# Kernel optimization log

Measured on AMD Instinct MI355X. Metric: run time of the kernel, lower is better.

Reference implementation:

```python
import jax, jax.numpy as jnp
import numpy as np

B, N, S, D1, D2 = 8, 8192, 2048, 128, 256
MLP = [256, 128]
IN_CH = D1 + D2
EPS_INTERP = 1e-8
EPS_BN = 1e-5


def setup_inputs() -> dict:
    key = jax.random.key(0)
    ks = jax.random.split(key, 12)
    inp = {
        "xyz1": jax.random.normal(ks[0], (B, 3, N), dtype=jnp.float32),
        "xyz2": jax.random.normal(ks[1], (B, 3, S), dtype=jnp.float32),
        "points1": jax.random.normal(ks[2], (B, D1, N), dtype=jnp.float32),
        "points2": jax.random.normal(ks[3], (B, D2, S), dtype=jnp.float32),
    }
    # Conv1d(k=1) weights are [out, in]; BN has gamma/beta per channel.
    last = IN_CH
    for i, oc in enumerate(MLP):
        inp[f"W{i}"] = jax.random.normal(ks[4 + 2 * i], (oc, last), dtype=jnp.float32) * (1.0 / np.sqrt(last))
        inp[f"b{i}"] = jnp.zeros((oc,), dtype=jnp.float32)
        inp[f"g{i}"] = jnp.ones((oc,), dtype=jnp.float32)
        inp[f"be{i}"] = jnp.zeros((oc,), dtype=jnp.float32)
        last = oc
    return inp


def _interpolate(xyz1, xyz2, points2):
    # xyz1: [B,3,N] -> [B,N,3]; xyz2: [B,3,S] -> [B,S,3]; points2: [B,D2,S] -> [B,S,D2]
    x1 = jnp.transpose(xyz1, (0, 2, 1))
    x2 = jnp.transpose(xyz2, (0, 2, 1))
    p2 = jnp.transpose(points2, (0, 2, 1))
    # squared distances [B,N,S]
    dists = (jnp.sum(x1 * x1, -1)[:, :, None]
             - 2.0 * jnp.einsum("bnc,bsc->bns", x1, x2)
             + jnp.sum(x2 * x2, -1)[:, None, :])
    neg_d, idx = jax.lax.top_k(-dists, 3)         # 3 nearest neighbors
    d = -neg_d                                     # [B,N,3]
    recip = 1.0 / (d + EPS_INTERP)
    weight = recip / jnp.sum(recip, axis=2, keepdims=True)
    gathered = jax.vmap(lambda p, i: p[i])(p2, idx)   # [B,N,3,D2]
    return jnp.sum(gathered * weight[..., None], axis=2)  # [B,N,D2]


def _conv_bn_relu(x, W, b, g, be):
    # x: [B,C,N]; 1x1 conv == channel GEMM
    y = jnp.einsum("oc,bcn->bon", W, x) + b[None, :, None]
    mean = jnp.mean(y, axis=(0, 2), keepdims=True)
    var = jnp.mean((y - mean) ** 2, axis=(0, 2), keepdims=True)  # biased, torch BN train
    y = (y - mean) * jax.lax.rsqrt(var + EPS_BN)
    y = y * g[None, :, None] + be[None, :, None]
    return jax.nn.relu(y)


def reference(xyz1, xyz2, points1, points2, W0, b0, g0, be0, W1, b1, g1, be1):
    interp = _interpolate(xyz1, xyz2, points2)               # [B,N,D2]
    p1 = jnp.transpose(points1, (0, 2, 1))                    # [B,N,D1]
    new_points = jnp.concatenate([p1, interp], axis=-1)       # [B,N,D1+D2]
    new_points = jnp.transpose(new_points, (0, 2, 1))         # [B,D1+D2,N]
    new_points = _conv_bn_relu(new_points, W0, b0, g0, be0)
    new_points = _conv_bn_relu(new_points, W1, b1, g1, be1)
    return new_points
```

## Files before the change

### kernel.cpp

```cpp
#include <hip/hip_runtime.h>

typedef unsigned short ushort_t;
typedef __bf16 bf16x8 __attribute__((ext_vector_type(8)));
typedef float floatx4 __attribute__((ext_vector_type(4)));

#define B_ 8
#define N_ 8192
#define S_ 2048
#define D1_ 128
#define D2_ 256
#define INCH_ 384
#define M_ 65536
#define G2_NBLK 512

#define ASYNC_CP16(g, l)                                                  \
  __builtin_amdgcn_global_load_lds(                                       \
      (const __attribute__((address_space(1))) void*)(g),                 \
      (__attribute__((address_space(3))) void*)(l), 16, 0, 0)

constexpr size_t OFF_STATS = 0;
constexpr size_t OFF_W0B   = 8192;
constexpr size_t OFF_W1B   = 204800;
constexpr size_t OFF_X2P   = 270336;
constexpr size_t OFF_P2T   = 532480;
constexpr size_t OFF_XC    = 8921088;
constexpr size_t OFF_Y1    = 59252736;

__device__ __forceinline__ ushort_t f2bf(float f) {
  __bf16 h = (__bf16)f;
  union { __bf16 h; ushort_t u; } v;
  v.h = h;
  return v.u;
}
__device__ __forceinline__ float bf2f(ushort_t h) {
  return __uint_as_float(((unsigned int)h) << 16);
}

__device__ __forceinline__ void ins3(float e, int s,
                                     float& c0, float& c1, float& c2,
                                     int& i0, int& i1, int& i2) {
  bool l0 = e < c0, l1 = e < c1, l2 = e < c2;
  float nf0 = fminf(e, c0);
  float nf1 = __builtin_amdgcn_fmed3f(e, c0, c1);
  float nf2 = __builtin_amdgcn_fmed3f(e, c1, c2);
  i2 = l1 ? i1 : (l2 ? s : i2);
  i1 = l0 ? i0 : (l1 ? s : i1);
  i0 = l0 ? s : i0;
  c0 = nf0; c1 = nf1; c2 = nf2;
}

__global__ __launch_bounds__(256) void k_prep(const float* __restrict__ W0,
                                              const float* __restrict__ W1,
                                              const float* __restrict__ xyz2,
                                              ushort_t* __restrict__ W0b,
                                              ushort_t* __restrict__ W1b,
                                              float4* __restrict__ x2p) {
  int i = blockIdx.x * 256 + threadIdx.x;
  if (i < 98304) {
    W0b[i] = f2bf(W0[i]);
  } else if (i < 131072) {
    W1b[i - 98304] = f2bf(W1[i - 98304]);
  } else {
    int idx = i - 131072;
    int b = idx >> 11, s = idx & (S_ - 1);
    const float* base = xyz2 + (size_t)b * 3 * S_;
    float x = base[s], y = base[S_ + s], z = base[2 * S_ + s];
    x2p[idx] = make_float4(x, y, z, 0.5f * (x * x + y * y + z * z));
  }
}

__global__ void k_tr_p2(const float* __restrict__ P2, ushort_t* __restrict__ p2t) {
  __shared__ float t[32][33];
  int b = blockIdx.z;
  int s0 = blockIdx.x * 32;
  int c0 = blockIdx.y * 32;
  int tx = threadIdx.x, ty = threadIdx.y;
#pragma unroll
  for (int j = 0; j < 4; j++) {
    int c = c0 + ty + j * 8;
    t[ty + j * 8][tx] = P2[((size_t)b * D2_ + c) * S_ + s0 + tx];
  }
  __syncthreads();
#pragma unroll
  for (int j = 0; j < 4; j++) {
    int s = s0 + ty + j * 8;
    p2t[((size_t)b * S_ + s) * D2_ + c0 + tx] = f2bf(t[tx][ty + j * 8]);
  }
}

__global__ void k_tr_p1(const float* __restrict__ P1, ushort_t* __restrict__ Xc) {
  __shared__ float t[32][33];
  int b = blockIdx.z;
  int n0 = blockIdx.x * 32;
  int c0 = blockIdx.y * 32;
  int tx = threadIdx.x, ty = threadIdx.y;
#pragma unroll
  for (int j = 0; j < 4; j++) {
    int c = c0 + ty + j * 8;
    t[ty + j * 8][tx] = P1[((size_t)b * D1_ + c) * N_ + n0 + tx];
  }
  __syncthreads();
#pragma unroll
  for (int j = 0; j < 4; j++) {
    int n = n0 + ty + j * 8;
    Xc[((size_t)b * N_ + n) * INCH_ + c0 + tx] = f2bf(t[tx][ty + j * 8]);
  }
}

__global__ __launch_bounds__(512, 8) void k_knn(const float* __restrict__ xyz1,
                                                const float4* __restrict__ x2p,
                                                const ushort_t* __restrict__ p2t,
                                                ushort_t* __restrict__ Xc) {
  __shared__ float4 xs[8 * 289];
  __shared__ float wsh[64 * 3];
  __shared__ int   ish[64 * 3];
  int t = threadIdx.x;
  int q0 = blockIdx.x * 64;
  int b = q0 >> 13;
  int n0 = q0 & (N_ - 1);
  for (int l = t; l < S_; l += 512)
    xs[(l >> 8) * 289 + (l & 255)] = x2p[(size_t)b * S_ + l];
  int sub = t & 7;
  int qg = t >> 3;
  int n = n0 + qg;
  float qx = xyz1[((size_t)b * 3 + 0) * N_ + n];
  float qy = xyz1[((size_t)b * 3 + 1) * N_ + n];
  float qz = xyz1[((size_t)b * 3 + 2) * N_ + n];
  float nrm1 = qx * qx + qy * qy + qz * qz;
  __syncthreads();
  const float4* bp = xs + sub * 289;
  float k0 = 3e38f, k1 = 3e38f, k2 = 3e38f, k3 = 3e38f;
#pragma unroll 4
  for (int i = 0; i < 256; ++i) {
    float4 P = bp[i];
    float e = fmaf(-qx, P.x, fmaf(-qy, P.y, fmaf(-qz, P.z, P.w)));
    float dd = fmaf(2.f, e, nrm1);
    unsigned int kb = (__float_as_uint(dd) & 0xFFFFFF00u) | (unsigned int)i;
    float k = __uint_as_float(kb);
    float n0_ = fminf(k, k0);
    float n1_ = __builtin_amdgcn_fmed3f(k, k0, k1);
    float n2_ = __builtin_amdgcn_fmed3f(k, k1, k2);
    float n3_ = __builtin_amdgcn_fmed3f(k, k2, k3);
    k0 = n0_; k1 = n1_; k2 = n2_; k3 = n3_;
  }
  float ed[4];
  int   si[4];
  {
    float kk[4] = {k0, k1, k2, k3};
#pragma unroll
    for (int c = 0; c < 4; ++c) {
      int loc = (int)(__float_as_uint(kk[c]) & 255u);
      float4 P = bp[loc];
      float e = fmaf(-qx, P.x, fmaf(-qy, P.y, fmaf(-qz, P.z, P.w)));
      ed[c] = fmaf(2.f, e, nrm1);
      si[c] = (sub << 8) + loc;
    }
  }
  float c0 = 3e38f, c1 = 3e38f, c2 = 3e38f;
  int i0 = 0, i1 = 0, i2 = 0;
#pragma unroll
  for (int c = 0; c < 4; ++c) ins3(ed[c], si[c], c0, c1, c2, i0, i1, i2);
#pragma unroll
  for (int d = 1; d < 8; d <<= 1) {
    float e0 = __shfl_xor(c0, d); int s0 = __shfl_xor(i0, d);
    float e1 = __shfl_xor(c1, d); int s1 = __shfl_xor(i1, d);
    float e2 = __shfl_xor(c2, d); int s2 = __shfl_xor(i2, d);
    ins3(e0, s0, c0, c1, c2, i0, i1, i2);
    ins3(e1, s1, c0, c1, c2, i0, i1, i2);
    ins3(e2, s2, c0, c1, c2, i0, i1, i2);
  }
  if (sub == 0) {
    float r0 = 1.f / (c0 + 1e-8f);
    float r1 = 1.f / (c1 + 1e-8f);
    float r2 = 1.f / (c2 + 1e-8f);
    float rs = 1.f / (r0 + r1 + r2);
    wsh[qg * 3 + 0] = r0 * rs; wsh[qg * 3 + 1] = r1 * rs; wsh[qg * 3 + 2] = r2 * rs;
    ish[qg * 3 + 0] = i0; ish[qg * 3 + 1] = i1; ish[qg * 3 + 2] = i2;
  }
  __syncthreads();
  int lane = t & 63, grp = t >> 6;
  size_t sbase2 = (size_t)b * S_;
#pragma unroll 2
  for (int it = 0; it < 8; ++it) {
    int ql = it * 8 + grp;
    int q = q0 + ql;
    float w0 = wsh[ql * 3 + 0], w1 = wsh[ql * 3 + 1], w2 = wsh[ql * 3 + 2];
    int j0 = ish[ql * 3 + 0], j1 = ish[ql * 3 + 1], j2 = ish[ql * 3 + 2];
    ushort4 a0 = *(const ushort4*)&p2t[(sbase2 + j0) * D2_ + lane * 4];
    ushort4 a1 = *(const ushort4*)&p2t[(sbase2 + j1) * D2_ + lane * 4];
    ushort4 a2 = *(const ushort4*)&p2t[(sbase2 + j2) * D2_ + lane * 4];
    ushort4 o;
    o.x = f2bf(w0 * bf2f(a0.x) + w1 * bf2f(a1.x) + w2 * bf2f(a2.x));
    o.y = f2bf(w0 * bf2f(a0.y) + w1 * bf2f(a1.y) + w2 * bf2f(a2.y));
    o.z = f2bf(w0 * bf2f(a0.z) + w1 * bf2f(a1.z) + w2 * bf2f(a2.z));
    o.w = f2bf(w0 * bf2f(a0.w) + w1 * bf2f(a1.w) + w2 * bf2f(a2.w));
    *(ushort4*)&Xc[(size_t)q * INCH_ + D1_ + lane * 4] = o;
  }
}

__global__ __launch_bounds__(512) void k_gemm1(const ushort_t* __restrict__ A,
                                               const ushort_t* __restrict__ Bw,
                                               ushort_t* __restrict__ Cc,
                                               float* __restrict__ sum,
                                               float* __restrict__ ssq) {
  __shared__ __align__(16) ushort_t As[128 * 32];
  __shared__ __align__(16) ushort_t Bs[256 * 32];
  const int tid = threadIdx.x;
  const int m0 = blockIdx.x * 128;
  const int wave = tid >> 6;
  const int wuni = __builtin_amdgcn_readfirstlane(wave);
  const int lane = tid & 63;
  const int quad = lane >> 4;
  const int l16 = lane & 15;
  const int wrow = (wave >> 2) * 64;
  const int wcol = (wave & 3) * 64;
  const int arow = tid >> 2, aseg = tid & 3;
  floatx4 acc[4][4];
#pragma unroll
  for (int i = 0; i < 4; i++)
#pragma unroll
    for (int j = 0; j < 4; j++) acc[i][j] = (floatx4){0.f, 0.f, 0.f, 0.f};

  for (int k0 = 0; k0 < INCH_; k0 += 32) {
    ASYNC_CP16(&A[(size_t)(m0 + arow) * INCH_ + k0 + aseg * 8], &As[wuni * 512]);
#pragma unroll
    for (int it = 0; it < 2; it++) {
      int l = tid + it * 512;
      int row = l >> 2, seg = l & 3;
      ASYNC_CP16(&Bw[(size_t)row * INCH_ + k0 + seg * 8], &Bs[it * 4096 + wuni * 512]);
    }
    __syncthreads();
    bf16x8 af[4], bfr[4];
#pragma unroll
    for (int mt = 0; mt < 4; mt++) af[mt] = *(const bf16x8*)&As[(wrow + mt * 16 + l16) * 32 + quad * 8];
#pragma unroll
    for (int nt = 0; nt < 4; nt++) bfr[nt] = *(const bf16x8*)&Bs[(wcol + nt * 16 + l16) * 32 + quad * 8];
#pragma unroll
    for (int mt = 0; mt < 4; mt++)
#pragma unroll
      for (int nt = 0; nt < 4; nt++)
        acc[mt][nt] = __builtin_amdgcn_mfma_f32_16x16x32_bf16(af[mt], bfr[nt], acc[mt][nt], 0, 0, 0);
    __syncthreads();
  }
#pragma unroll
  for (int mt = 0; mt < 4; mt++) {
#pragma unroll
    for (int i = 0; i < 4; i++) {
      int row = m0 + wrow + mt * 16 + quad * 4 + i;
#pragma unroll
      for (int nt = 0; nt < 4; nt++) {
        int col = wcol + nt * 16 + l16;
        Cc[(size_t)row * 256 + col] = f2bf(acc[mt][nt][i]);
      }
    }
  }
#pragma unroll
  for (int nt = 0; nt < 4; nt++) {
    float s = 0.f, s2 = 0.f;
#pragma unroll
    for (int mt = 0; mt < 4; mt++)
#pragma unroll
      for (int i = 0; i < 4; i++) {
        float v = acc[mt][nt][i];
        s += v;
        s2 = fmaf(v, v, s2);
      }
    s += __shfl_xor(s, 16);  s2 += __shfl_xor(s2, 16);
    s += __shfl_xor(s, 32);  s2 += __shfl_xor(s2, 32);
    if (quad == 0) {
      int col = wcol + nt * 16 + l16;
      atomicAdd(&sum[col], s);
      atomicAdd(&ssq[col], s2);
    }
  }
}

__global__ __launch_bounds__(256, 2) void k_gemm2o(const ushort_t* __restrict__ Y1,
                                                   const ushort_t* __restrict__ Bw,
                                                   const float* __restrict__ sum0,
                                                   const float* __restrict__ ssq0,
                                                   const float* __restrict__ g0,
                                                   const float* __restrict__ be0,
                                                   const float* __restrict__ g1,
                                                   const float* __restrict__ be1,
                                                   float* __restrict__ sum1,
                                                   float* __restrict__ ssq1,
                                                   unsigned int* __restrict__ barcnt,
                                                   float* __restrict__ out) {
  __shared__ __align__(16) char ubuf[64 * 129 * 4];
  __shared__ float scs[256], shs[256];
  ushort_t* As = (ushort_t*)ubuf;
  ushort_t* Bs = (ushort_t*)(ubuf + 8192);
  float* tb = (float*)ubuf;
  const int tid = threadIdx.x;
  const int m0 = blockIdx.x * 128;
  const int b = m0 >> 13;
  const int n0 = m0 & (N_ - 1);
  const int wave = tid >> 6;
  const int wuni = __builtin_amdgcn_readfirstlane(wave);
  const int lane = tid & 63;
  const int quad = lane >> 4;
  const int l16 = lane & 15;
  const int wrow = (wave >> 1) * 64;
  const int wcol = (wave & 1) * 64;
  {
    float mean = sum0[tid] * (1.f / 65536.f);
    float var = ssq0[tid] * (1.f / 65536.f) - mean * mean;
    float sc = rsqrtf(var + 1e-5f) * g0[tid];
    scs[tid] = sc;
    shs[tid] = be0[tid] - mean * sc;
  }
  floatx4 acc[4][4];
#pragma unroll
  for (int i = 0; i < 4; i++)
#pragma unroll
    for (int j = 0; j < 4; j++) acc[i][j] = (floatx4){0.f, 0.f, 0.f, 0.f};
  __syncthreads();

  for (int k0 = 0; k0 < 256; k0 += 32) {
#pragma unroll
    for (int it = 0; it < 2; it++) {
      int l = tid + it * 256;
      int row = l >> 2, seg = l & 3;
      ASYNC_CP16(&Bw[(size_t)row * 256 + k0 + seg * 8], &Bs[it * 2048 + wuni * 512]);
    }
#pragma unroll
    for (int it = 0; it < 2; it++) {
      int l = tid + it * 256;
      int row = l >> 2, seg = l & 3;
      ushort4 y01 = *(const ushort4*)&Y1[(size_t)(m0 + row) * 256 + k0 + seg * 8];
      ushort4 y23 = *(const ushort4*)&Y1[(size_t)(m0 + row) * 256 + k0 + seg * 8 + 4];
      int c = k0 + seg * 8;
      ushort4 o0, o1;
      o0.x = f2bf(fmaxf(fmaf(bf2f(y01.x), scs[c + 0], shs[c + 0]), 0.f));
      o0.y = f2bf(fmaxf(fmaf(bf2f(y01.y), scs[c + 1], shs[c + 1]), 0.f));
      o0.z = f2bf(fmaxf(fmaf(bf2f(y01.z), scs[c + 2], shs[c + 2]), 0.f));
      o0.w = f2bf(fmaxf(fmaf(bf2f(y01.w), scs[c + 3], shs[c + 3]), 0.f));
      o1.x = f2bf(fmaxf(fmaf(bf2f(y23.x), scs[c + 4], shs[c + 4]), 0.f));
      o1.y = f2bf(fmaxf(fmaf(bf2f(y23.y), scs[c + 5], shs[c + 5]), 0.f));
      o1.z = f2bf(fmaxf(fmaf(bf2f(y23.z), scs[c + 6], shs[c + 6]), 0.f));
      o1.w = f2bf(fmaxf(fmaf(bf2f(y23.w), scs[c + 7], shs[c + 7]), 0.f));
      *(ushort4*)&As[row * 32 + seg * 8] = o0;
      *(ushort4*)&As[row * 32 + seg * 8 + 4] = o1;
    }
    __syncthreads();
    bf16x8 af[4], bfr[4];
#pragma unroll
    for (int mt = 0; mt < 4; mt++) af[mt] = *(const bf16x8*)&As[(wrow + mt * 16 + l16) * 32 + quad * 8];
#pragma unroll
    for (int nt = 0; nt < 4; nt++) bfr[nt] = *(const bf16x8*)&Bs[(wcol + nt * 16 + l16) * 32 + quad * 8];
#pragma unroll
    for (int mt = 0; mt < 4; mt++)
#pragma unroll
      for (int nt = 0; nt < 4; nt++)
        acc[mt][nt] = __builtin_amdgcn_mfma_f32_16x16x32_bf16(af[mt], bfr[nt], acc[mt][nt], 0, 0, 0);
    __syncthreads();
  }
#pragma unroll
  for (int nt = 0; nt < 4; nt++) {
    float s = 0.f, s2 = 0.f;
#pragma unroll
    for (int mt = 0; mt < 4; mt++)
#pragma unroll
      for (int i = 0; i < 4; i++) {
        float v = acc[mt][nt][i];
        s += v;
        s2 = fmaf(v, v, s2);
      }
    s += __shfl_xor(s, 16);  s2 += __shfl_xor(s2, 16);
    s += __shfl_xor(s, 32);  s2 += __shfl_xor(s2, 32);
    if (quad == 0) {
      int col = wcol + nt * 16 + l16;
      atomicAdd(&sum1[col], s);
      atomicAdd(&ssq1[col], s2);
    }
  }

  __syncthreads();
  if (tid == 0) {
    __hip_atomic_fetch_add(barcnt, 1u, __ATOMIC_ACQ_REL, __HIP_MEMORY_SCOPE_AGENT);
    while (__hip_atomic_load(barcnt, __ATOMIC_ACQUIRE, __HIP_MEMORY_SCOPE_AGENT)
           < (unsigned)G2_NBLK) {
      __builtin_amdgcn_s_sleep(8);
    }
  }
  __syncthreads();

  if (tid < 128) {
    float sv = __hip_atomic_load(&sum1[tid], __ATOMIC_RELAXED, __HIP_MEMORY_SCOPE_AGENT);
    float qv = __hip_atomic_load(&ssq1[tid], __ATOMIC_RELAXED, __HIP_MEMORY_SCOPE_AGENT);
    float mean = sv * (1.f / 65536.f);
    float var = qv * (1.f / 65536.f) - mean * mean;
    float sc = rsqrtf(var + 1e-5f) * g1[tid];
    scs[tid] = sc;
    shs[tid] = be1[tid] - mean * sc;
  }
  __syncthreads();

  const int mych = wrow >> 6;
#pragma unroll
  for (int c2 = 0; c2 < 2; ++c2) {
    if (mych == c2) {
#pragma unroll
      for (int mt = 0; mt < 4; mt++)
#pragma unroll
        for (int i = 0; i < 4; i++) {
          int rl = mt * 16 + quad * 4 + i;
#pragma unroll
          for (int nt = 0; nt < 4; nt++) {
            int col = wcol + nt * 16 + l16;
            float v = fmaxf(fmaf(acc[mt][nt][i], scs[col], shs[col]), 0.f);
            tb[rl * 129 + col] = v;
          }
        }
    }
    __syncthreads();
#pragma unroll
    for (int it = 0; it < 32; ++it) {
      int idx = it * 256 + tid;
      int j = idx & 63, c = idx >> 6;
      out[((size_t)(b * 128 + c)) * N_ + n0 + c2 * 64 + j] = tb[j * 129 + c];
    }
    __syncthreads();
  }
}

extern "C" void kernel_launch(void* const* d_in, const int* in_sizes, int n_in,
                              void* d_out, int out_size, void* d_ws, size_t ws_size,
                              hipStream_t stream) {
  const float* xyz1    = (const float*)d_in[0];
  const float* xyz2    = (const float*)d_in[1];
  const float* points1 = (const float*)d_in[2];
  const float* points2 = (const float*)d_in[3];
  const float* W0 = (const float*)d_in[4];
  const float* g0 = (const float*)d_in[6];
  const float* be0 = (const float*)d_in[7];
  const float* W1 = (const float*)d_in[8];
  const float* g1 = (const float*)d_in[10];
  const float* be1 = (const float*)d_in[11];
  float* out = (float*)d_out;
  char* ws = (char*)d_ws;

  float* sum0   = (float*)(ws + OFF_STATS);
  float* ssq0   = sum0 + 256;
  float* sum1   = sum0 + 512;
  float* ssq1   = sum0 + 640;
  unsigned int* barcnt = (unsigned int*)(sum0 + 768);
  ushort_t* W0b = (ushort_t*)(ws + OFF_W0B);
  ushort_t* W1b = (ushort_t*)(ws + OFF_W1B);
  float4* x2p   = (float4*)(ws + OFF_X2P);
  ushort_t* p2t = (ushort_t*)(ws + OFF_P2T);
  ushort_t* Xc  = (ushort_t*)(ws + OFF_XC);
  ushort_t* Y1b = (ushort_t*)(ws + OFF_Y1);

  hipMemsetAsync(ws + OFF_STATS, 0, 6144, stream);
  k_prep<<<576, 256, 0, stream>>>(W0, W1, xyz2, W0b, W1b, x2p);
  k_tr_p2<<<dim3(64, 8, 8), dim3(32, 8), 0, stream>>>(points2, p2t);
  k_tr_p1<<<dim3(256, 4, 8), dim3(32, 8), 0, stream>>>(points1, Xc);
  k_knn<<<1024, 512, 0, stream>>>(xyz1, x2p, p2t, Xc);
  k_gemm1<<<512, 512, 0, stream>>>(Xc, W0b, Y1b, sum0, ssq0);
  k_gemm2o<<<G2_NBLK, 256, 0, stream>>>(Y1b, W1b, sum0, ssq0, g0, be0,
                                        g1, be1, sum1, ssq1, barcnt, out);
}
```

Baseline: 269.4 us.

## Replace in-kernel grid barrier with separate BN-apply kernel and smaller GEMM tiles

The second GEMM no longer spins on a global atomic barrier to get the final BN statistics. It writes pre-BN results as a transposed bf16 buffer (reusing the Xc workspace), and a new elementwise kernel applies BN and ReLU to produce the fp32 output. GEMM tiles are halved to 64 rows with 1024 blocks and launch bounds raised for occupancy. This removes the barrier wait and the co-residency requirement, but adds a bf16 intermediate round trip through global memory, an extra launch, and an extra bf16 rounding before BN.

```diff
diff --git a/kernel.cpp b/kernel.cpp
--- a/kernel.cpp
+++ b/kernel.cpp
@@ -11,7 +11,6 @@
 #define D2_ 256
 #define INCH_ 384
 #define M_ 65536
-#define G2_NBLK 512
 
 #define ASYNC_CP16(g, l)                                                  \
   __builtin_amdgcn_global_load_lds(                                       \
@@ -275,25 +274,22 @@
   }
 }
 
-__global__ __launch_bounds__(256, 2) void k_gemm2o(const ushort_t* __restrict__ Y1,
+__global__ __launch_bounds__(256, 4) void k_gemm2t(const ushort_t* __restrict__ Y1,
                                                    const ushort_t* __restrict__ Bw,
                                                    const float* __restrict__ sum0,
                                                    const float* __restrict__ ssq0,
                                                    const float* __restrict__ g0,
                                                    const float* __restrict__ be0,
-                                                   const float* __restrict__ g1,
-                                                   const float* __restrict__ be1,
+                                                   ushort_t* __restrict__ Y2t,
                                                    float* __restrict__ sum1,
-                                                   float* __restrict__ ssq1,
-                                                   unsigned int* __restrict__ barcnt,
-                                                   float* __restrict__ out) {
+                                                   float* __restrict__ ssq1) {
   __shared__ __align__(16) char ubuf[64 * 129 * 4];
   __shared__ float scs[256], shs[256];
   ushort_t* As = (ushort_t*)ubuf;
-  ushort_t* Bs = (ushort_t*)(ubuf + 8192);
+  ushort_t* Bs = (ushort_t*)(ubuf + 4096);
   float* tb = (float*)ubuf;
   const int tid = threadIdx.x;
-  const int m0 = blockIdx.x * 128;
+  const int m0 = blockIdx.x * 64;
   const int b = m0 >> 13;
   const int n0 = m0 & (N_ - 1);
   const int wave = tid >> 6;
@@ -301,7 +297,7 @@
   const int lane = tid & 63;
   const int quad = lane >> 4;
   const int l16 = lane & 15;
-  const int wrow = (wave >> 1) * 64;
+  const int wrow = (wave >> 1) * 32;
   const int wcol = (wave & 1) * 64;
   {
     float mean = sum0[tid] * (1.f / 65536.f);
@@ -310,13 +306,14 @@
     scs[tid] = sc;
     shs[tid] = be0[tid] - mean * sc;
   }
-  floatx4 acc[4][4];
-#pragma unroll
-  for (int i = 0; i < 4; i++)
+  floatx4 acc[2][4];
+#pragma unroll
+  for (int i = 0; i < 2; i++)
 #pragma unroll
     for (int j = 0; j < 4; j++) acc[i][j] = (floatx4){0.f, 0.f, 0.f, 0.f};
   __syncthreads();
 
+  const int arow = tid >> 2, aseg = tid & 3;
   for (int k0 = 0; k0 < 256; k0 += 32) {
 #pragma unroll
     for (int it = 0; it < 2; it++) {
@@ -324,13 +321,10 @@
       int row = l >> 2, seg = l & 3;
       ASYNC_CP16(&Bw[(size_t)row * 256 + k0 + seg * 8], &Bs[it * 2048 + wuni * 512]);
     }
-#pragma unroll
-    for (int it = 0; it < 2; it++) {
-      int l = tid + it * 256;
-      int row = l >> 2, seg = l & 3;
-      ushort4 y01 = *(const ushort4*)&Y1[(size_t)(m0 + row) * 256 + k0 + seg * 8];
-      ushort4 y23 = *(const ushort4*)&Y1[(size_t)(m0 + row) * 256 + k0 + seg * 8 + 4];
-      int c = k0 + seg * 8;
+    {
+      ushort4 y01 = *(const ushort4*)&Y1[(size_t)(m0 + arow) * 256 + k0 + aseg * 8];
+      ushort4 y23 = *(const ushort4*)&Y1[(size_t)(m0 + arow) * 256 + k0 + aseg * 8 + 4];
+      int c = k0 + aseg * 8;
       ushort4 o0, o1;
       o0.x = f2bf(fmaxf(fmaf(bf2f(y01.x), scs[c + 0], shs[c + 0]), 0.f));
       o0.y = f2bf(fmaxf(fmaf(bf2f(y01.y), scs[c + 1], shs[c + 1]), 0.f));
@@ -340,17 +334,17 @@
       o1.y = f2bf(fmaxf(fmaf(bf2f(y23.y), scs[c + 5], shs[c + 5]), 0.f));
       o1.z = f2bf(fmaxf(fmaf(bf2f(y23.z), scs[c + 6], shs[c + 6]), 0.f));
       o1.w = f2bf(fmaxf(fmaf(bf2f(y23.w), scs[c + 7], shs[c + 7]), 0.f));
-      *(ushort4*)&As[row * 32 + seg * 8] = o0;
-      *(ushort4*)&As[row * 32 + seg * 8 + 4] = o1;
+      *(ushort4*)&As[arow * 32 + aseg * 8] = o0;
+      *(ushort4*)&As[arow * 32 + aseg * 8 + 4] = o1;
     }
     __syncthreads();
-    bf16x8 af[4], bfr[4];
-#pragma unroll
-    for (int mt = 0; mt < 4; mt++) af[mt] = *(const bf16x8*)&As[(wrow + mt * 16 + l16) * 32 + quad * 8];
+    bf16x8 af[2], bfr[4];
+#pragma unroll
+    for (int mt = 0; mt < 2; mt++) af[mt] = *(const bf16x8*)&As[(wrow + mt * 16 + l16) * 32 + quad * 8];
 #pragma unroll
     for (int nt = 0; nt < 4; nt++) bfr[nt] = *(const bf16x8*)&Bs[(wcol + nt * 16 + l16) * 32 + quad * 8];
 #pragma unroll
-    for (int mt = 0; mt < 4; mt++)
+    for (int mt = 0; mt < 2; mt++)
 #pragma unroll
       for (int nt = 0; nt < 4; nt++)
         acc[mt][nt] = __builtin_amdgcn_mfma_f32_16x16x32_bf16(af[mt], bfr[nt], acc[mt][nt], 0, 0, 0);
@@ -360,7 +354,7 @@
   for (int nt = 0; nt < 4; nt++) {
     float s = 0.f, s2 = 0.f;
 #pragma unroll
-    for (int mt = 0; mt < 4; mt++)
+    for (int mt = 0; mt < 2; mt++)
 #pragma unroll
       for (int i = 0; i < 4; i++) {
         float v = acc[mt][nt][i];
@@ -375,53 +369,62 @@
       atomicAdd(&ssq1[col], s2);
     }
   }
-
-  __syncthreads();
-  if (tid == 0) {
-    __hip_atomic_fetch_add(barcnt, 1u, __ATOMIC_ACQ_REL, __HIP_MEMORY_SCOPE_AGENT);
-    while (__hip_atomic_load(barcnt, __ATOMIC_ACQUIRE, __HIP_MEMORY_SCOPE_AGENT)
-           < (unsigned)G2_NBLK) {
-      __builtin_amdgcn_s_sleep(8);
-    }
-  }
-  __syncthreads();
-
+#pragma unroll
+  for (int mt = 0; mt < 2; mt++)
+#pragma unroll
+    for (int i = 0; i < 4; i++) {
+      int rl = wrow + mt * 16 + quad * 4 + i;
+#pragma unroll
+      for (int nt = 0; nt < 4; nt++) {
+        int col = wcol + nt * 16 + l16;
+        tb[rl * 129 + col] = acc[mt][nt][i];
+      }
+    }
+  __syncthreads();
+#pragma unroll
+  for (int it = 0; it < 8; ++it) {
+    int idx = it * 256 + tid;
+    int c = idx >> 4;
+    int j4 = (idx & 15) * 4;
+    ushort4 v;
+    v.x = f2bf(tb[(j4 + 0) * 129 + c]);
+    v.y = f2bf(tb[(j4 + 1) * 129 + c]);
+    v.z = f2bf(tb[(j4 + 2) * 129 + c]);
+    v.w = f2bf(tb[(j4 + 3) * 129 + c]);
+    *(ushort4*)&Y2t[((size_t)(b * 128 + c)) * N_ + n0 + j4] = v;
+  }
+}
+
+__global__ __launch_bounds__(256) void k_out2(const ushort_t* __restrict__ Y2t,
+                                              const float* __restrict__ sum1,
+                                              const float* __restrict__ ssq1,
+                                              const float* __restrict__ g1,
+                                              const float* __restrict__ be1,
+                                              float* __restrict__ out) {
+  __shared__ float sc1[128], sh1[128];
+  int tid = threadIdx.x;
   if (tid < 128) {
-    float sv = __hip_atomic_load(&sum1[tid], __ATOMIC_RELAXED, __HIP_MEMORY_SCOPE_AGENT);
-    float qv = __hip_atomic_load(&ssq1[tid], __ATOMIC_RELAXED, __HIP_MEMORY_SCOPE_AGENT);
-    float mean = sv * (1.f / 65536.f);
-    float var = qv * (1.f / 65536.f) - mean * mean;
+    float mean = sum1[tid] * (1.f / 65536.f);
+    float var = ssq1[tid] * (1.f / 65536.f) - mean * mean;
     float sc = rsqrtf(var + 1e-5f) * g1[tid];
-    scs[tid] = sc;
-    shs[tid] = be1[tid] - mean * sc;
-  }
-  __syncthreads();
-
-  const int mych = wrow >> 6;
-#pragma unroll
-  for (int c2 = 0; c2 < 2; ++c2) {
-    if (mych == c2) {
-#pragma unroll
-      for (int mt = 0; mt < 4; mt++)
-#pragma unroll
-        for (int i = 0; i < 4; i++) {
-          int rl = mt * 16 + quad * 4 + i;
-#pragma unroll
-          for (int nt = 0; nt < 4; nt++) {
-            int col = wcol + nt * 16 + l16;
-            float v = fmaxf(fmaf(acc[mt][nt][i], scs[col], shs[col]), 0.f);
-            tb[rl * 129 + col] = v;
-          }
-        }
-    }
-    __syncthreads();
-#pragma unroll
-    for (int it = 0; it < 32; ++it) {
-      int idx = it * 256 + tid;
-      int j = idx & 63, c = idx >> 6;
-      out[((size_t)(b * 128 + c)) * N_ + n0 + c2 * 64 + j] = tb[j * 129 + c];
-    }
-    __syncthreads();
+    sc1[tid] = sc;
+    sh1[tid] = be1[tid] - mean * sc;
+  }
+  __syncthreads();
+#pragma unroll
+  for (int it = 0; it < 4; ++it) {
+    int fid = (it * 2048 + blockIdx.x) * 256 + tid;
+    int r = fid >> 11;
+    int c = r & 127;
+    int n4 = (fid & 2047) * 4;
+    ushort4 y = *(const ushort4*)&Y2t[((size_t)r << 13) + n4];
+    float sc = sc1[c], sh = sh1[c];
+    float4 v;
+    v.x = fmaxf(fmaf(bf2f(y.x), sc, sh), 0.f);
+    v.y = fmaxf(fmaf(bf2f(y.y), sc, sh), 0.f);
+    v.z = fmaxf(fmaf(bf2f(y.z), sc, sh), 0.f);
+    v.w = fmaxf(fmaf(bf2f(y.w), sc, sh), 0.f);
+    *(float4*)&out[((size_t)r << 13) + n4] = v;
   }
 }
 
@@ -445,13 +448,13 @@
   float* ssq0   = sum0 + 256;
   float* sum1   = sum0 + 512;
   float* ssq1   = sum0 + 640;
-  unsigned int* barcnt = (unsigned int*)(sum0 + 768);
   ushort_t* W0b = (ushort_t*)(ws + OFF_W0B);
   ushort_t* W1b = (ushort_t*)(ws + OFF_W1B);
   float4* x2p   = (float4*)(ws + OFF_X2P);
   ushort_t* p2t = (ushort_t*)(ws + OFF_P2T);
   ushort_t* Xc  = (ushort_t*)(ws + OFF_XC);
   ushort_t* Y1b = (ushort_t*)(ws + OFF_Y1);
+  ushort_t* Y2t = (ushort_t*)(ws + OFF_XC);
 
   hipMemsetAsync(ws + OFF_STATS, 0, 6144, stream);
   k_prep<<<576, 256, 0, stream>>>(W0, W1, xyz2, W0b, W1b, x2p);
@@ -459,6 +462,7 @@
   k_tr_p1<<<dim3(256, 4, 8), dim3(32, 8), 0, stream>>>(points1, Xc);
   k_knn<<<1024, 512, 0, stream>>>(xyz1, x2p, p2t, Xc);
   k_gemm1<<<512, 512, 0, stream>>>(Xc, W0b, Y1b, sum0, ssq0);
-  k_gemm2o<<<G2_NBLK, 256, 0, stream>>>(Y1b, W1b, sum0, ssq0, g0, be0,
-                                        g1, be1, sum1, ssq1, barcnt, out);
-}
+  k_gemm2t<<<1024, 256, 0, stream>>>(Y1b, W1b, sum0, ssq0, g0, be0,
+                                     Y2t, sum1, ssq1);
+  k_out2<<<2048, 256, 0, stream>>>(Y2t, sum1, ssq1, g1, be1, out);
+}
```

After: 279.5 us. 3.7% more time.
